# Kernel tuning notes

Hardware: AMD Instinct MI355X
Metric: run time of the kernel (lower is better)

## Reference

```python
import jax, jax.numpy as jnp
import numpy as np

LN_EPS = 1e-5

def layer_norm(x, w, b):
    mu = jnp.mean(x, axis=-1, keepdims=True)
    var = jnp.mean(jnp.square(x - mu), axis=-1, keepdims=True)
    return (x - mu) * jax.lax.rsqrt(var + LN_EPS) * w + b

def adaptive_mask_np(aa, bb, ada_para=0.2):
    # True = disallowed (matches torch ~bool mask). Static shapes -> numpy.
    adaptive_num = int(bb * ada_para)
    cc = bb // aa
    i = np.arange(aa)
    start = i * cc
    end = start + cc + adaptive_num
    over = end > bb - 1
    start = np.where(over, np.maximum(start - (end - (bb - 1)), 0), start)
    end = np.where(over, bb, end)
    cols = np.arange(bb)
    allowed = (cols[None, :] >= start[:, None]) & (cols[None, :] < end[:, None])
    return jnp.asarray(~allowed)  # [aa, bb] bool

def setup_inputs() -> dict:
    key = jax.random.key(0)
    ks = jax.random.split(key, 20)
    Lq, Lk, B, d, dff = 512, 4096, 4, 512, 2048
    s = lambda k, shape: jax.random.normal(k, shape, dtype=jnp.float32) * 0.02
    inp = {
        'tgt': jax.random.normal(ks[0], (Lq, B, d), dtype=jnp.float32),
        'memory': jax.random.normal(ks[1], (Lk, B, d), dtype=jnp.float32),
        'Wq': s(ks[2], (d, d)), 'bq': jnp.zeros((d,), jnp.float32),
        'Wk': s(ks[3], (d, d)), 'bk': jnp.zeros((d,), jnp.float32),
        'Wv': s(ks[4], (d, d)), 'bv': jnp.zeros((d,), jnp.float32),
        'Wo': s(ks[5], (d, d)), 'bo': jnp.zeros((d,), jnp.float32),
        'W1': s(ks[6], (dff, d)), 'b1': jnp.zeros((dff,), jnp.float32),
        'W2': s(ks[7], (d, dff)), 'b2': jnp.zeros((d,), jnp.float32),
        'ln1_w': jnp.ones((d,), jnp.float32), 'ln1_b': jnp.zeros((d,), jnp.float32),
        'ln2_w': jnp.ones((d,), jnp.float32), 'ln2_b': jnp.zeros((d,), jnp.float32),
        'ln3_w': jnp.ones((d,), jnp.float32), 'ln3_b': jnp.zeros((d,), jnp.float32),
        'ln4_w': jnp.ones((d,), jnp.float32), 'ln4_b': jnp.zeros((d,), jnp.float32),
    }
    return inp

def reference(tgt, memory, Wq, bq, Wk, bk, Wv, bv, Wo, bo, W1, b1, W2, b2,
              ln1_w, ln1_b, ln2_w, ln2_b, ln3_w, ln3_b, ln4_w, ln4_b):
    Lq, B, d = tgt.shape
    Lk = memory.shape[0]
    H = 8
    hd = d // H
    scale = 1.0 / jnp.sqrt(jnp.asarray(hd, tgt.dtype))

    t = layer_norm(tgt, ln1_w, ln1_b)      # [Lq,B,d]
    m = layer_norm(memory, ln2_w, ln2_b)   # [Lk,B,d]

    mask = adaptive_mask_np(Lq, Lk, 0.2)   # [Lq,Lk] bool, True=masked

    q = (t @ Wq.T + bq).reshape(Lq, B, H, hd)
    k = (m @ Wk.T + bk).reshape(Lk, B, H, hd)
    v = (m @ Wv.T + bv).reshape(Lk, B, H, hd)

    scores = jnp.einsum('qbhd,kbhd->bhqk', q * scale, k)
    scores = jnp.where(mask[None, None], -jnp.inf, scores)
    p = jax.nn.softmax(scores, axis=-1)                   # [B,H,Lq,Lk]
    attn_weights = jnp.mean(p, axis=1)                    # [B,Lq,Lk] (avg over heads)

    ctx = jnp.einsum('bhqk,kbhd->qbhd', p, v).reshape(Lq, B, d)
    tgt2 = ctx @ Wo.T + bo

    x = t + tgt2                       # dropout1 = identity (eval)
    x = layer_norm(x, ln3_w, ln3_b)
    ff = jax.nn.relu(x @ W1.T + b1) @ W2.T + b2
    x = x + ff                         # dropout2 = identity (eval)
    x = layer_norm(x, ln4_w, ln4_b)
    return (x, attn_weights)
```

## Files before the change

### kernel.cpp

```cpp
#include <hip/hip_runtime.h>
#include <hip/hip_bf16.h>

typedef __hip_bfloat16 bf16_t;
typedef __bf16 bf16x8 __attribute__((ext_vector_type(8)));
typedef float f32x4 __attribute__((ext_vector_type(4)));

#define LQ 512
#define LK 4096
#define BATCH 4
#define DMODEL 512
#define NHEAD 8
#define HEADDIM 64
#define DFF 2048
#define LN_EPS 1e-5f

#define KSTR 2080
#define VSTR 4128

__device__ inline float tofl(float x) { return x; }
__device__ inline float tofl(bf16_t x) { return __bfloat162float(x); }
__device__ inline void stfl(float* p, float v) { *p = v; }
__device__ inline void stfl(bf16_t* p, float v) { *p = __float2bfloat16(v); }

__device__ __forceinline__ void gld_lds16(const bf16_t* g, void* lds_base) {
    __builtin_amdgcn_global_load_lds(
        (const __attribute__((address_space(1))) uint32_t*)g,
        (__attribute__((address_space(3))) uint32_t*)lds_base, 16, 0, 0);
}

__global__ void prep_kernel(const float* __restrict__ s0, const float* __restrict__ s1,
                            const float* __restrict__ s2, const float* __restrict__ s3,
                            const float* __restrict__ s4,
                            bf16_t* __restrict__ wqkvo, bf16_t* __restrict__ w1bf) {
    int t = blockIdx.x * 256 + threadIdx.x;
    int which = t >> 16;
    int idx = (t & 65535) * 4;
    const float* s; bf16_t* d;
    if (which < 4) {
        s = (which == 0 ? s0 : which == 1 ? s1 : which == 2 ? s2 : s3);
        d = wqkvo + (size_t)which * 262144;
    } else {
        s = s4 + (size_t)(which - 4) * 262144;
        d = w1bf + (size_t)(which - 4) * 262144;
    }
    float4 v = *(const float4*)(s + idx);
    d[idx + 0] = __float2bfloat16(v.x);
    d[idx + 1] = __float2bfloat16(v.y);
    d[idx + 2] = __float2bfloat16(v.z);
    d[idx + 3] = __float2bfloat16(v.w);
}

__global__ void conv_w2(const float* __restrict__ s, bf16_t* __restrict__ d) {
    int i = (blockIdx.x * 256 + threadIdx.x) * 4;
    float4 v = *(const float4*)(s + i);
    d[i + 0] = __float2bfloat16(v.x);
    d[i + 1] = __float2bfloat16(v.y);
    d[i + 2] = __float2bfloat16(v.z);
    d[i + 3] = __float2bfloat16(v.w);
}

template <typename TOUT, bool DUAL>
__global__ void ln_kernel(const float* __restrict__ in, const float* __restrict__ w,
                          const float* __restrict__ b, TOUT* __restrict__ out1,
                          float* __restrict__ out2) {
    __shared__ float red[256];
    const int row = blockIdx.x;
    const int tid = threadIdx.x;
    const float* x = in + (size_t)row * DMODEL;
    float v0 = x[tid];
    float v1 = x[tid + 256];

    red[tid] = v0 + v1;
    __syncthreads();
    for (int s = 128; s > 0; s >>= 1) { if (tid < s) red[tid] += red[tid + s]; __syncthreads(); }
    float mu = red[0] * (1.0f / DMODEL);
    __syncthreads();

    float d0 = v0 - mu, d1 = v1 - mu;
    red[tid] = d0 * d0 + d1 * d1;
    __syncthreads();
    for (int s = 128; s > 0; s >>= 1) { if (tid < s) red[tid] += red[tid + s]; __syncthreads(); }
    float inv = rsqrtf(red[0] * (1.0f / DMODEL) + LN_EPS);

    float r0 = d0 * inv * w[tid] + b[tid];
    float r1 = d1 * inv * w[tid + 256] + b[tid + 256];
    TOUT* o = out1 + (size_t)row * DMODEL;
    stfl(&o[tid], r0);
    stfl(&o[tid + 256], r1);
    if (DUAL) {
        float* o2 = out2 + (size_t)row * DMODEL;
        o2[tid] = r0;
        o2[tid + 256] = r1;
    }
}

__global__ void ln12_kernel(const float* __restrict__ tgt, const float* __restrict__ memory,
                            const float* __restrict__ w1, const float* __restrict__ b1,
                            const float* __restrict__ w2, const float* __restrict__ b2,
                            bf16_t* __restrict__ t_bf, float* __restrict__ t_f32,
                            bf16_t* __restrict__ m_buf) {
    __shared__ float red[256];
    const int row = blockIdx.x;
    const int tid = threadIdx.x;
    const float* in; const float* w; const float* b;
    bf16_t* o1; float* o2; bool dual;
    if (row < 2048) {
        in = tgt + (size_t)row * DMODEL; w = w1; b = b1;
        o1 = t_bf + (size_t)row * DMODEL; o2 = t_f32 + (size_t)row * DMODEL; dual = true;
    } else {
        int r2 = row - 2048;
        in = memory + (size_t)r2 * DMODEL; w = w2; b = b2;
        o1 = m_buf + (size_t)r2 * DMODEL; o2 = nullptr; dual = false;
    }
    float v0 = in[tid];
    float v1 = in[tid + 256];
    red[tid] = v0 + v1;
    __syncthreads();
    for (int s = 128; s > 0; s >>= 1) { if (tid < s) red[tid] += red[tid + s]; __syncthreads(); }
    float mu = red[0] * (1.0f / DMODEL);
    __syncthreads();
    float d0 = v0 - mu, d1 = v1 - mu;
    red[tid] = d0 * d0 + d1 * d1;
    __syncthreads();
    for (int s = 128; s > 0; s >>= 1) { if (tid < s) red[tid] += red[tid + s]; __syncthreads(); }
    float inv = rsqrtf(red[0] * (1.0f / DMODEL) + LN_EPS);
    float r0 = d0 * inv * w[tid] + b[tid];
    float r1 = d1 * inv * w[tid + 256] + b[tid + 256];
    o1[tid] = __float2bfloat16(r0);
    o1[tid + 256] = __float2bfloat16(r1);
    if (dual) {
        o2[tid] = r0;
        o2[tid + 256] = r1;
    }
}

template <int TN, typename TC, bool RELU, bool RESID, bool KREMAP = false>
__global__ __launch_bounds__(256) void gemm_mfma(
        const bf16_t* __restrict__ A, const bf16_t* __restrict__ B,
        const float* __restrict__ bias, const float* __restrict__ resid,
        TC* __restrict__ C, int M, int N, int K) {
    __shared__ uint4 As4[1024];
    __shared__ uint4 Bs4[TN * 8];

    const int tid = threadIdx.x;
    const int lane = tid & 63;
    const int wave = tid >> 6;
    const int row16 = lane & 15;
    const int quad = lane >> 4;
    const int n0 = blockIdx.x * TN;
    const int m0 = blockIdx.y * 128;

    constexpr int MI = (TN == 128) ? 4 : 2;
    const int wy = (TN == 128) ? (wave >> 1) : wave;
    const int wx = (TN == 128) ? (wave & 1) : 0;
    const int m_base = wy * ((TN == 128) ? 64 : 32);
    const int n_base = wx * 64;

    const int rr = lane >> 3;
    const int kc = (lane & 7) ^ rr;
    const int kx = row16 & 7;

    const bf16_t* AsE = (const bf16_t*)As4;
    const bf16_t* BsE = (const bf16_t*)Bs4;

    f32x4 acc[MI][4] = {};

    for (int k0 = 0; k0 < K; k0 += 64) {
#pragma unroll
        for (int it = 0; it < 4; it++) {
            int issue = it * 4 + wave;
            int r = issue * 8 + rr;
            gld_lds16(A + (size_t)(m0 + r) * K + k0 + kc * 8, &As4[issue * 64]);
        }
#pragma unroll
        for (int it = 0; it < TN / 32; it++) {
            int issue = it * 4 + wave;
            int r = issue * 8 + rr;
            gld_lds16(B + (size_t)(n0 + r) * K + k0 + kc * 8, &Bs4[issue * 64]);
        }
        __syncthreads();
#pragma unroll
        for (int s = 0; s < 2; s++) {
            const int kq = s * 4 + quad;
            const int kcs = (kq ^ kx) * 8;
            bf16x8 af[MI], bfr[4];
#pragma unroll
            for (int i = 0; i < MI; i++)
                af[i] = *(const bf16x8*)&AsE[(m_base + i * 16 + row16) * 64 + kcs];
#pragma unroll
            for (int j = 0; j < 4; j++)
                bfr[j] = *(const bf16x8*)&BsE[(n_base + j * 16 + row16) * 64 + kcs];
#pragma unroll
            for (int i = 0; i < MI; i++)
#pragma unroll
                for (int j = 0; j < 4; j++)
                    acc[i][j] = __builtin_amdgcn_mfma_f32_16x16x32_bf16(af[i], bfr[j], acc[i][j], 0, 0, 0);
        }
        __syncthreads();
    }

#pragma unroll
    for (int i = 0; i < MI; i++) {
#pragma unroll
        for (int j = 0; j < 4; j++) {
            int col = n0 + n_base + j * 16 + row16;
            float bsv = bias[col];
#pragma unroll
            for (int r = 0; r < 4; r++) {
                int row = m0 + m_base + i * 16 + quad * 4 + r;
                float val = acc[i][j][r] + bsv;
                if (RESID) val += resid[(size_t)row * N + col];
                if (RELU) val = fmaxf(val, 0.0f);
                size_t caddr = KREMAP
                    ? ((size_t)(row >> 2) * KSTR + (size_t)(row & 3) * 512 + col)
                    : ((size_t)row * N + col);
                stfl(&C[caddr], val);
            }
        }
    }
}

__global__ __launch_bounds__(256) void transpose_kv(const bf16_t* __restrict__ kb,
                                                    bf16_t* __restrict__ kT) {
    __shared__ bf16_t tile[64][80];
    const int kt = blockIdx.x * 64;
    const int ct = blockIdx.y * 64;
    const int b  = blockIdx.z;
    const int t = threadIdx.x;
    {
        int kl = t >> 2, cl = (t & 3) * 16;
        const bf16_t* src = kb + ((size_t)(kt + kl) * 4 + b) * 512 + ct + cl;
        *(uint4*)&tile[kl][cl]     = *(const uint4*)src;
        *(uint4*)&tile[kl][cl + 8] = *(const uint4*)(src + 8);
    }
    __syncthreads();
    {
        int cl2 = t >> 2, ks = (t & 3) * 16;
        __attribute__((aligned(16))) bf16_t vals[16];
#pragma unroll
        for (int j = 0; j < 16; j++) vals[j] = tile[ks + j][cl2];
        bf16_t* dst = kT + ((size_t)b * 512 + ct + cl2) * VSTR + kt + ks;
        *(uint4*)dst       = *(const uint4*)&vals[0];
        *(uint4*)(dst + 8) = *(const uint4*)&vals[8];
    }
}

__device__ __forceinline__ void qk_issue(const bf16_t* kb_base, int us, int g,
                                         int row16, bf16x8 (&b0)[8], bf16x8 (&b1)[8]) {
#pragma unroll
    for (int j = 0; j < 8; ++j) {
        int key = us + (g * 8 + j) * 16 + row16;
        int key_eff = key > 4095 ? 4095 : key;
        const bf16_t* kr = kb_base + (size_t)key_eff * KSTR;
        b0[j] = *(const bf16x8*)kr;
        b1[j] = *(const bf16x8*)(kr + 32);
    }
}

__device__ __forceinline__ void qk_compute(int g, bf16x8 (&b0)[8], bf16x8 (&b1)[8],
        const bf16x8 aq0, const bf16x8 aq1, float (&l)[4], bf16_t* PsH,
        int row16, int quad, const int (&sq)[4], const int (&eq)[4], int us) {
#pragma unroll
    for (int j = 0; j < 8; ++j) {
        int it = g * 8 + j;
        f32x4 acc = {};
        acc = __builtin_amdgcn_mfma_f32_16x16x32_bf16(aq0, b0[j], acc, 0, 0, 0);
        acc = __builtin_amdgcn_mfma_f32_16x16x32_bf16(aq1, b1[j], acc, 0, 0, 0);
        int key = us + it * 16 + row16;
#pragma unroll
        for (int r = 0; r < 4; r++) {
            int ql = quad * 4 + r;
            bool valid = (key >= sq[r]) && (key < eq[r]);
            float p = valid ? __expf(0.125f * acc[r]) : 0.0f;
            l[r] += p;
            if (ql < 8) PsH[ql * 904 + it * 16 + row16] = __float2bfloat16(p);
        }
    }
}

__device__ __forceinline__ void pv_issue(const bf16_t* vbase, int g, int row16, int quad,
                                         bf16x8 (&vb)[4][4]) {
#pragma unroll
    for (int j = 0; j < 4; ++j) {
        int it = g * 4 + j;
#pragma unroll
        for (int nt = 0; nt < 4; ++nt)
            vb[j][nt] = *(const bf16x8*)(vbase + (size_t)(nt * 16 + row16) * VSTR
                                         + it * 32 + quad * 8);
    }
}

__device__ __forceinline__ void pv_compute(int g, bf16x8 (&vb)[4][4], const bf16_t* PsH,
        const bf16_t* Zrow, int row16, int quad, f32x4 (&o)[4]) {
#pragma unroll
    for (int j = 0; j < 4; ++j) {
        int it = g * 4 + j;
        const bf16_t* ap_src = (row16 < 8) ? &PsH[row16 * 904 + it * 32 + quad * 8]
                                           : &Zrow[0];
        bf16x8 ap = *(const bf16x8*)ap_src;
#pragma unroll
        for (int nt = 0; nt < 4; ++nt)
            o[nt] = __builtin_amdgcn_mfma_f32_16x16x32_bf16(ap, vb[j][nt], o[nt], 0, 0, 0);
    }
}

__global__ __launch_bounds__(512, 1) void attn_mfma(
        const bf16_t* __restrict__ qb,
        const bf16_t* __restrict__ kb,
        const bf16_t* __restrict__ vT,
        bf16_t* __restrict__ ctx,
        float* __restrict__ attn_out) {
    extern __shared__ char smem[];
    bf16_t* Ps   = (bf16_t*)smem;
    bf16_t* Qs   = (bf16_t*)(smem + 115712);
    bf16_t* Zrow = (bf16_t*)(smem + 115712 + 8320);
    float*  Ls   = (float*)(smem + 115712 + 8320 + 1808);

    const int blk = blockIdx.x;
    const int b  = (blk & 7) >> 1;
    const int qt = ((blk >> 3) << 1) | (blk & 1);
    const int q0 = qt * 8;
    const int tid = threadIdx.x;
    const int lane = tid & 63;
    const int h = tid >> 6;
    const int hoffg = h * HEADDIM;
    const int row16 = lane & 15;
    const int quad = lane >> 4;

    int us; { int s = q0 * 8, e = s + 827; if (e > 4095) s = 3268; us = s; }
    int sq[4], eq[4];
#pragma unroll
    for (int r = 0; r < 4; r++) {
        int ql = quad * 4 + r;
        if (ql < 8) {
            int s = (q0 + ql) * 8, e = s + 827;
            if (e > 4095) { s = 3268; e = 4096; }
            sq[r] = s; eq[r] = e;
        } else { sq[r] = 0; eq[r] = 0; }
    }

    {
        int r = tid >> 6, coff = (tid & 63) * 8;
        *(uint4*)&Qs[r * 520 + coff] =
            *(const uint4*)(qb + ((size_t)(q0 + r) * 4 + b) * 512 + coff);
        if (tid < 113) { uint4 z = {0, 0, 0, 0}; *(uint4*)&Zrow[tid * 8] = z; }
    }
    __syncthreads();

    const bf16_t* q0p = (row16 < 8) ? &Qs[row16 * 520 + hoffg + quad * 8] : &Zrow[0];
    const bf16_t* q1p = (row16 < 8) ? &Qs[row16 * 520 + hoffg + 32 + quad * 8] : &Zrow[8];
    const bf16x8 aq0 = *(const bf16x8*)q0p;
    const bf16x8 aq1 = *(const bf16x8*)q1p;

    bf16_t* PsH = Ps + h * 8 * 904;
    const bf16_t* kb_base = kb + b * 512 + hoffg + quad * 8;

    bf16x8 ka0[8], ka1[8], kc0[8], kc1[8];
    float l[4] = {0.f, 0.f, 0.f, 0.f};
    qk_issue(kb_base, us, 0, row16, ka0, ka1);
    for (int gg = 0; gg < 3; ++gg) {
        qk_issue(kb_base, us, 2 * gg + 1, row16, kc0, kc1);
        qk_compute(2 * gg, ka0, ka1, aq0, aq1, l, PsH, row16, quad, sq, eq, us);
        qk_issue(kb_base, us, 2 * gg + 2, row16, ka0, ka1);
        qk_compute(2 * gg + 1, kc0, kc1, aq0, aq1, l, PsH, row16, quad, sq, eq, us);
    }
    bf16x8 va[4][4], vb_[4][4];
    const bf16_t* vbase = vT + (size_t)(b * 512 + hoffg) * VSTR + us;
    pv_issue(vbase, 0, row16, quad, va);
    qk_compute(6, ka0, ka1, aq0, aq1, l, PsH, row16, quad, sq, eq, us);

#pragma unroll
    for (int off = 1; off < 16; off <<= 1) {
#pragma unroll
        for (int r = 0; r < 4; r++) l[r] += __shfl_xor(l[r], off, 64);
    }
    float linv[4];
#pragma unroll
    for (int r = 0; r < 4; r++) linv[r] = 1.0f / l[r];
    if (row16 == 0) {
#pragma unroll
        for (int r = 0; r < 4; r++) {
            int ql = quad * 4 + r;
            if (ql < 8) Ls[h * 8 + ql] = linv[r];
        }
    }

    f32x4 o[4] = {};
    for (int gg = 0; gg < 3; ++gg) {
        pv_issue(vbase, 2 * gg + 1, row16, quad, vb_);
        pv_compute(2 * gg, va, PsH, Zrow, row16, quad, o);
        pv_issue(vbase, 2 * gg + 2, row16, quad, va);
        pv_compute(2 * gg + 1, vb_, PsH, Zrow, row16, quad, o);
    }
    pv_compute(6, va, PsH, Zrow, row16, quad, o);

    __syncthreads();

    {
        int qq = h;
        float ls[8];
#pragma unroll
        for (int hh = 0; hh < 8; ++hh) ls[hh] = 0.125f * Ls[hh * 8 + qq];
        float* rowp = attn_out + ((size_t)b * LQ + q0 + qq) * LK;
        const bf16_t* ps = Ps + qq * 904;
        for (int it = 0; it < 16; ++it) {
            int c4 = (it * 64 + lane) * 4;
            float4 v = {0.f, 0.f, 0.f, 0.f};
            int off = c4 - us;
            if (off >= -3 && off < 896) {
#pragma unroll
                for (int e = 0; e < 4; ++e) {
                    int pc = off + e;
                    float s = 0.f;
                    if (pc >= 0 && pc < 896) {
#pragma unroll
                        for (int hh = 0; hh < 8; ++hh)
                            s += ls[hh] * tofl(ps[hh * 8 * 904 + pc]);
                    }
                    (&v.x)[e] = s;
                }
            }
            *(float4*)(rowp + c4) = v;
        }
    }

#pragma unroll
    for (int nt = 0; nt < 4; nt++) {
#pragma unroll
        for (int r = 0; r < 4; r++) {
            int ql = quad * 4 + r;
            if (ql < 8) {
                ctx[((size_t)(q0 + ql) * 4 + b) * 512 + hoffg + nt * 16 + row16] =
                    __float2bfloat16(o[nt][r] * linv[r]);
            }
        }
    }
}

extern "C" void kernel_launch(void* const* d_in, const int* in_sizes, int n_in,
                              void* d_out, int out_size, void* d_ws, size_t ws_size,
                              hipStream_t stream) {
    const float* tgt    = (const float*)d_in[0];
    const float* memory = (const float*)d_in[1];
    const float* Wq = (const float*)d_in[2];
    const float* bq = (const float*)d_in[3];
    const float* Wk = (const float*)d_in[4];
    const float* bk = (const float*)d_in[5];
    const float* Wv = (const float*)d_in[6];
    const float* bv = (const float*)d_in[7];
    const float* Wo = (const float*)d_in[8];
    const float* bo = (const float*)d_in[9];
    const float* W1 = (const float*)d_in[10];
    const float* b1 = (const float*)d_in[11];
    const float* W2 = (const float*)d_in[12];
    const float* b2 = (const float*)d_in[13];
    const float* ln1w = (const float*)d_in[14];
    const float* ln1b = (const float*)d_in[15];
    const float* ln2w = (const float*)d_in[16];
    const float* ln2b = (const float*)d_in[17];
    const float* ln3w = (const float*)d_in[18];
    const float* ln3b = (const float*)d_in[19];
    const float* ln4w = (const float*)d_in[20];
    const float* ln4b = (const float*)d_in[21];

    const size_t M1 = (size_t)LQ * BATCH;
    const size_t M2 = (size_t)LK * BATCH;
    const size_t SZ1 = M1 * DMODEL;

    char* wsb = (char*)d_ws;
    const size_t MB = 1 << 20;
    bf16_t* m_buf   = (bf16_t*)(wsb + 0 * MB);
    bf16_t* vT_buf  = (bf16_t*)(wsb + 0 * MB);
    bf16_t* h_buf   = (bf16_t*)(wsb + 0 * MB);
    bf16_t* k_buf   = (bf16_t*)(wsb + 17 * MB);
    float*  xres    = (float*)(wsb + 17 * MB);
    float*  xln_f   = (float*)(wsb + 21 * MB);
    float*  x2_buf  = (float*)(wsb + 25 * MB);
    bf16_t* W2_bf   = (bf16_t*)(wsb + 34 * MB);
    bf16_t* v_buf   = (bf16_t*)(wsb + 34 * MB);
    bf16_t* t_bf    = (bf16_t*)(wsb + 50 * MB);
    bf16_t* xln_bf  = (bf16_t*)(wsb + 50 * MB);
    float*  t_f32   = (float*)(wsb + 52 * MB);
    bf16_t* q_bf    = (bf16_t*)(wsb + 56 * MB);
    bf16_t* ctx_buf = (bf16_t*)(wsb + 58 * MB);
    bf16_t* wqkvo   = (bf16_t*)(wsb + 60 * MB);
    bf16_t* W1_bf   = (bf16_t*)(wsb + 62 * MB);

    bf16_t* Wq_bf = wqkvo;
    bf16_t* Wk_bf = wqkvo + 262144;
    bf16_t* Wv_bf = wqkvo + 2 * 262144;
    bf16_t* Wo_bf = wqkvo + 3 * 262144;

    float* out_x    = (float*)d_out;
    float* out_attn = out_x + SZ1;

    prep_kernel<<<dim3(2048), dim3(256), 0, stream>>>(
        Wq, Wk, Wv, Wo, W1, wqkvo, W1_bf);

    ln12_kernel<<<dim3(M1 + M2), dim3(256), 0, stream>>>(
        tgt, memory, ln1w, ln1b, ln2w, ln2b, t_bf, t_f32, m_buf);

    gemm_mfma<64, bf16_t, false, false><<<dim3(8, 16), dim3(256), 0, stream>>>(
        t_bf, Wq_bf, bq, nullptr, q_bf, M1, DMODEL, DMODEL);
    gemm_mfma<128, bf16_t, false, false, true><<<dim3(4, 128), dim3(256), 0, stream>>>(
        m_buf, Wk_bf, bk, nullptr, k_buf, M2, DMODEL, DMODEL);
    gemm_mfma<128, bf16_t, false, false><<<dim3(4, 128), dim3(256), 0, stream>>>(
        m_buf, Wv_bf, bv, nullptr, v_buf, M2, DMODEL, DMODEL);

    transpose_kv<<<dim3(64, 8, 4), dim3(256), 0, stream>>>(v_buf, vT_buf);

    conv_w2<<<dim3(1024), dim3(256), 0, stream>>>(W2, W2_bf);

    const int attn_lds = 115712 + 8320 + 1808 + 256;
    hipFuncSetAttribute((const void*)attn_mfma,
                        hipFuncAttributeMaxDynamicSharedMemorySize, attn_lds);
    attn_mfma<<<dim3(256), dim3(512), attn_lds, stream>>>(
        q_bf, k_buf, vT_buf, ctx_buf, out_attn);

    gemm_mfma<64, float, false, true><<<dim3(8, 16), dim3(256), 0, stream>>>(
        ctx_buf, Wo_bf, bo, t_f32, xres, M1, DMODEL, DMODEL);

    ln_kernel<bf16_t, true><<<dim3(M1), dim3(256), 0, stream>>>(xres, ln3w, ln3b, xln_bf, xln_f);

    gemm_mfma<128, bf16_t, true, false><<<dim3(16, 16), dim3(256), 0, stream>>>(
        xln_bf, W1_bf, b1, nullptr, h_buf, M1, DFF, DMODEL);

    gemm_mfma<64, float, false, true><<<dim3(8, 16), dim3(256), 0, stream>>>(
        h_buf, W2_bf, b2, xln_f, x2_buf, M1, DMODEL, DFF);

    ln_kernel<float, false><<<dim3(M1), dim3(256), 0, stream>>>(x2_buf, ln4w, ln4b, out_x, nullptr);
}
```

Measured before the change: 305.8 us.

## Fuse K and V projections into one GEMM and triple-buffer attention loads

Replaces the two separate K and V projection GEMM launches with one kernel. It loads each A tile of the normalized memory once and computes both K and V outputs from it, which halves the A-side global traffic and removes one launch. The attention kernel also moves from double to triple buffering of K and V register fragments, issuing loads two stages ahead to hide more latency. The cost is higher register pressure in both kernels (two accumulator sets in the GEMM, three fragment buffers in attention), which could reduce occupancy or cause spills.

```diff
diff --git a/kernel.cpp b/kernel.cpp
--- a/kernel.cpp
+++ b/kernel.cpp
@@ -220,6 +220,101 @@
     }
 }
 
+__global__ __launch_bounds__(256, 1) void gemm_kv(
+        const bf16_t* __restrict__ A, const bf16_t* __restrict__ BK,
+        const bf16_t* __restrict__ BV, const float* __restrict__ biask,
+        const float* __restrict__ biasv, bf16_t* __restrict__ CK,
+        bf16_t* __restrict__ CV, int M, int N, int K) {
+    __shared__ uint4 As4[1024];
+    __shared__ uint4 BKs4[1024];
+    __shared__ uint4 BVs4[1024];
+
+    const int tid = threadIdx.x;
+    const int lane = tid & 63;
+    const int wave = tid >> 6;
+    const int row16 = lane & 15;
+    const int quad = lane >> 4;
+    const int n0 = blockIdx.x * 128;
+    const int m0 = blockIdx.y * 128;
+
+    const int wy = wave >> 1;
+    const int wx = wave & 1;
+    const int m_base = wy * 64;
+    const int n_base = wx * 64;
+
+    const int rr = lane >> 3;
+    const int kc = (lane & 7) ^ rr;
+    const int kx = row16 & 7;
+
+    const bf16_t* AsE = (const bf16_t*)As4;
+    const bf16_t* BKsE = (const bf16_t*)BKs4;
+    const bf16_t* BVsE = (const bf16_t*)BVs4;
+
+    f32x4 accK[4][4] = {};
+    f32x4 accV[4][4] = {};
+
+    for (int k0 = 0; k0 < K; k0 += 64) {
+#pragma unroll
+        for (int it = 0; it < 4; it++) {
+            int issue = it * 4 + wave;
+            int r = issue * 8 + rr;
+            gld_lds16(A + (size_t)(m0 + r) * K + k0 + kc * 8, &As4[issue * 64]);
+        }
+#pragma unroll
+        for (int it = 0; it < 4; it++) {
+            int issue = it * 4 + wave;
+            int r = issue * 8 + rr;
+            gld_lds16(BK + (size_t)(n0 + r) * K + k0 + kc * 8, &BKs4[issue * 64]);
+        }
+#pragma unroll
+        for (int it = 0; it < 4; it++) {
+            int issue = it * 4 + wave;
+            int r = issue * 8 + rr;
+            gld_lds16(BV + (size_t)(n0 + r) * K + k0 + kc * 8, &BVs4[issue * 64]);
+        }
+        __syncthreads();
+#pragma unroll
+        for (int s = 0; s < 2; s++) {
+            const int kq = s * 4 + quad;
+            const int kcs = (kq ^ kx) * 8;
+            bf16x8 af[4], bkf[4], bvf[4];
+#pragma unroll
+            for (int i = 0; i < 4; i++)
+                af[i] = *(const bf16x8*)&AsE[(m_base + i * 16 + row16) * 64 + kcs];
+#pragma unroll
+            for (int j = 0; j < 4; j++) {
+                bkf[j] = *(const bf16x8*)&BKsE[(n_base + j * 16 + row16) * 64 + kcs];
+                bvf[j] = *(const bf16x8*)&BVsE[(n_base + j * 16 + row16) * 64 + kcs];
+            }
+#pragma unroll
+            for (int i = 0; i < 4; i++)
+#pragma unroll
+                for (int j = 0; j < 4; j++) {
+                    accK[i][j] = __builtin_amdgcn_mfma_f32_16x16x32_bf16(af[i], bkf[j], accK[i][j], 0, 0, 0);
+                    accV[i][j] = __builtin_amdgcn_mfma_f32_16x16x32_bf16(af[i], bvf[j], accV[i][j], 0, 0, 0);
+                }
+        }
+        __syncthreads();
+    }
+
+#pragma unroll
+    for (int i = 0; i < 4; i++) {
+#pragma unroll
+        for (int j = 0; j < 4; j++) {
+            int col = n0 + n_base + j * 16 + row16;
+            float bk_ = biask[col];
+            float bv_ = biasv[col];
+#pragma unroll
+            for (int r = 0; r < 4; r++) {
+                int row = m0 + m_base + i * 16 + quad * 4 + r;
+                CK[(size_t)(row >> 2) * KSTR + (size_t)(row & 3) * 512 + col] =
+                    __float2bfloat16(accK[i][j][r] + bk_);
+                CV[(size_t)row * N + col] = __float2bfloat16(accV[i][j][r] + bv_);
+            }
+        }
+    }
+}
+
 __global__ __launch_bounds__(256) void transpose_kv(const bf16_t* __restrict__ kb,
                                                     bf16_t* __restrict__ kT) {
     __shared__ bf16_t tile[64][80];
@@ -355,19 +450,27 @@
     bf16_t* PsH = Ps + h * 8 * 904;
     const bf16_t* kb_base = kb + b * 512 + hoffg + quad * 8;
 
-    bf16x8 ka0[8], ka1[8], kc0[8], kc1[8];
+    bf16x8 kA0[8], kA1[8], kB0[8], kB1[8], kC0[8], kC1[8];
     float l[4] = {0.f, 0.f, 0.f, 0.f};
-    qk_issue(kb_base, us, 0, row16, ka0, ka1);
-    for (int gg = 0; gg < 3; ++gg) {
-        qk_issue(kb_base, us, 2 * gg + 1, row16, kc0, kc1);
-        qk_compute(2 * gg, ka0, ka1, aq0, aq1, l, PsH, row16, quad, sq, eq, us);
-        qk_issue(kb_base, us, 2 * gg + 2, row16, ka0, ka1);
-        qk_compute(2 * gg + 1, kc0, kc1, aq0, aq1, l, PsH, row16, quad, sq, eq, us);
-    }
-    bf16x8 va[4][4], vb_[4][4];
+    qk_issue(kb_base, us, 0, row16, kA0, kA1);
+    qk_issue(kb_base, us, 1, row16, kB0, kB1);
+    qk_compute(0, kA0, kA1, aq0, aq1, l, PsH, row16, quad, sq, eq, us);
+    qk_issue(kb_base, us, 2, row16, kC0, kC1);
+    qk_compute(1, kB0, kB1, aq0, aq1, l, PsH, row16, quad, sq, eq, us);
+    qk_issue(kb_base, us, 3, row16, kA0, kA1);
+    qk_compute(2, kC0, kC1, aq0, aq1, l, PsH, row16, quad, sq, eq, us);
+    qk_issue(kb_base, us, 4, row16, kB0, kB1);
+    qk_compute(3, kA0, kA1, aq0, aq1, l, PsH, row16, quad, sq, eq, us);
+    qk_issue(kb_base, us, 5, row16, kC0, kC1);
+    qk_compute(4, kB0, kB1, aq0, aq1, l, PsH, row16, quad, sq, eq, us);
+    qk_issue(kb_base, us, 6, row16, kA0, kA1);
+
+    bf16x8 vA[4][4], vB[4][4], vC[4][4];
     const bf16_t* vbase = vT + (size_t)(b * 512 + hoffg) * VSTR + us;
-    pv_issue(vbase, 0, row16, quad, va);
-    qk_compute(6, ka0, ka1, aq0, aq1, l, PsH, row16, quad, sq, eq, us);
+    pv_issue(vbase, 0, row16, quad, vA);
+    qk_compute(5, kC0, kC1, aq0, aq1, l, PsH, row16, quad, sq, eq, us);
+    pv_issue(vbase, 1, row16, quad, vB);
+    qk_compute(6, kA0, kA1, aq0, aq1, l, PsH, row16, quad, sq, eq, us);
 
 #pragma unroll
     for (int off = 1; off < 16; off <<= 1) {
@@ -386,13 +489,18 @@
     }
 
     f32x4 o[4] = {};
-    for (int gg = 0; gg < 3; ++gg) {
-        pv_issue(vbase, 2 * gg + 1, row16, quad, vb_);
-        pv_compute(2 * gg, va, PsH, Zrow, row16, quad, o);
-        pv_issue(vbase, 2 * gg + 2, row16, quad, va);
-        pv_compute(2 * gg + 1, vb_, PsH, Zrow, row16, quad, o);
-    }
-    pv_compute(6, va, PsH, Zrow, row16, quad, o);
+    pv_issue(vbase, 2, row16, quad, vC);
+    pv_compute(0, vA, PsH, Zrow, row16, quad, o);
+    pv_issue(vbase, 3, row16, quad, vA);
+    pv_compute(1, vB, PsH, Zrow, row16, quad, o);
+    pv_issue(vbase, 4, row16, quad, vB);
+    pv_compute(2, vC, PsH, Zrow, row16, quad, o);
+    pv_issue(vbase, 5, row16, quad, vC);
+    pv_compute(3, vA, PsH, Zrow, row16, quad, o);
+    pv_issue(vbase, 6, row16, quad, vA);
+    pv_compute(4, vB, PsH, Zrow, row16, quad, o);
+    pv_compute(5, vC, PsH, Zrow, row16, quad, o);
+    pv_compute(6, vA, PsH, Zrow, row16, quad, o);
 
     __syncthreads();
 
@@ -502,10 +610,9 @@
 
     gemm_mfma<64, bf16_t, false, false><<<dim3(8, 16), dim3(256), 0, stream>>>(
         t_bf, Wq_bf, bq, nullptr, q_bf, M1, DMODEL, DMODEL);
-    gemm_mfma<128, bf16_t, false, false, true><<<dim3(4, 128), dim3(256), 0, stream>>>(
-        m_buf, Wk_bf, bk, nullptr, k_buf, M2, DMODEL, DMODEL);
-    gemm_mfma<128, bf16_t, false, false><<<dim3(4, 128), dim3(256), 0, stream>>>(
-        m_buf, Wv_bf, bv, nullptr, v_buf, M2, DMODEL, DMODEL);
+
+    gemm_kv<<<dim3(4, 128), dim3(256), 0, stream>>>(
+        m_buf, Wk_bf, Wv_bf, bk, bv, k_buf, v_buf, M2, DMODEL, DMODEL);
 
     transpose_kv<<<dim3(64, 8, 4), dim3(256), 0, stream>>>(v_buf, vT_buf);
 
```

Result: slower. 379.1 us (+23.9%).

## Add 64x64-tile GEMM for small projections and raise MFMA priority in attention

Applied to the files above, without the earlier changes.

Adds a new gemm64 kernel with 64x64 output tiles, so the Q, output-projection and W2 GEMMs (M=2048) launch 256 blocks instead of 128 and use more of the GPU's compute units. It also wraps the QK and PV MFMA compute sections of the attention kernel in s_setprio(1)/s_setprio(0), so waves doing matrix math get scheduling priority over waves issuing loads. The smaller tiles mean less data reuse per block and more loads of A and B overall.

```diff
diff --git a/kernel.cpp b/kernel.cpp
--- a/kernel.cpp
+++ b/kernel.cpp
@@ -220,6 +220,88 @@
     }
 }
 
+template <typename TC, bool RELU, bool RESID>
+__global__ __launch_bounds__(256) void gemm64(
+        const bf16_t* __restrict__ A, const bf16_t* __restrict__ B,
+        const float* __restrict__ bias, const float* __restrict__ resid,
+        TC* __restrict__ C, int M, int N, int K) {
+    __shared__ uint4 As4[512];
+    __shared__ uint4 Bs4[512];
+
+    const int tid = threadIdx.x;
+    const int lane = tid & 63;
+    const int wave = tid >> 6;
+    const int row16 = lane & 15;
+    const int quad = lane >> 4;
+    const int n0 = blockIdx.x * 64;
+    const int m0 = blockIdx.y * 64;
+
+    const int wy = wave >> 1;
+    const int wx = wave & 1;
+    const int m_base = wy * 32;
+    const int n_base = wx * 32;
+
+    const int rr = lane >> 3;
+    const int kc = (lane & 7) ^ rr;
+    const int kx = row16 & 7;
+
+    const bf16_t* AsE = (const bf16_t*)As4;
+    const bf16_t* BsE = (const bf16_t*)Bs4;
+
+    f32x4 acc[2][2] = {};
+
+    for (int k0 = 0; k0 < K; k0 += 64) {
+#pragma unroll
+        for (int it = 0; it < 2; it++) {
+            int issue = it * 4 + wave;
+            int r = issue * 8 + rr;
+            gld_lds16(A + (size_t)(m0 + r) * K + k0 + kc * 8, &As4[issue * 64]);
+        }
+#pragma unroll
+        for (int it = 0; it < 2; it++) {
+            int issue = it * 4 + wave;
+            int r = issue * 8 + rr;
+            gld_lds16(B + (size_t)(n0 + r) * K + k0 + kc * 8, &Bs4[issue * 64]);
+        }
+        __syncthreads();
+#pragma unroll
+        for (int s = 0; s < 2; s++) {
+            const int kq = s * 4 + quad;
+            const int kcs = (kq ^ kx) * 8;
+            bf16x8 af[2], bfr[2];
+#pragma unroll
+            for (int i = 0; i < 2; i++)
+                af[i] = *(const bf16x8*)&AsE[(m_base + i * 16 + row16) * 64 + kcs];
+#pragma unroll
+            for (int j = 0; j < 2; j++)
+                bfr[j] = *(const bf16x8*)&BsE[(n_base + j * 16 + row16) * 64 + kcs];
+#pragma unroll
+            for (int i = 0; i < 2; i++)
+#pragma unroll
+                for (int j = 0; j < 2; j++)
+                    acc[i][j] = __builtin_amdgcn_mfma_f32_16x16x32_bf16(af[i], bfr[j], acc[i][j], 0, 0, 0);
+        }
+        __syncthreads();
+    }
+
+#pragma unroll
+    for (int i = 0; i < 2; i++) {
+#pragma unroll
+        for (int j = 0; j < 2; j++) {
+            int col = n0 + n_base + j * 16 + row16;
+            float bsv = bias[col];
+#pragma unroll
+            for (int r = 0; r < 4; r++) {
+                int row = m0 + m_base + i * 16 + quad * 4 + r;
+                float val = acc[i][j][r] + bsv;
+                if (RESID) val += resid[(size_t)row * N + col];
+                if (RELU) val = fmaxf(val, 0.0f);
+                stfl(&C[(size_t)row * N + col], val);
+            }
+        }
+    }
+}
+
 __global__ __launch_bounds__(256) void transpose_kv(const bf16_t* __restrict__ kb,
                                                     bf16_t* __restrict__ kT) {
     __shared__ bf16_t tile[64][80];
@@ -260,6 +342,7 @@
 __device__ __forceinline__ void qk_compute(int g, bf16x8 (&b0)[8], bf16x8 (&b1)[8],
         const bf16x8 aq0, const bf16x8 aq1, float (&l)[4], bf16_t* PsH,
         int row16, int quad, const int (&sq)[4], const int (&eq)[4], int us) {
+    __builtin_amdgcn_s_setprio(1);
 #pragma unroll
     for (int j = 0; j < 8; ++j) {
         int it = g * 8 + j;
@@ -276,6 +359,7 @@
             if (ql < 8) PsH[ql * 904 + it * 16 + row16] = __float2bfloat16(p);
         }
     }
+    __builtin_amdgcn_s_setprio(0);
 }
 
 __device__ __forceinline__ void pv_issue(const bf16_t* vbase, int g, int row16, int quad,
@@ -292,6 +376,7 @@
 
 __device__ __forceinline__ void pv_compute(int g, bf16x8 (&vb)[4][4], const bf16_t* PsH,
         const bf16_t* Zrow, int row16, int quad, f32x4 (&o)[4]) {
+    __builtin_amdgcn_s_setprio(1);
 #pragma unroll
     for (int j = 0; j < 4; ++j) {
         int it = g * 4 + j;
@@ -302,6 +387,7 @@
         for (int nt = 0; nt < 4; ++nt)
             o[nt] = __builtin_amdgcn_mfma_f32_16x16x32_bf16(ap, vb[j][nt], o[nt], 0, 0, 0);
     }
+    __builtin_amdgcn_s_setprio(0);
 }
 
 __global__ __launch_bounds__(512, 1) void attn_mfma(
@@ -500,8 +586,9 @@
     ln12_kernel<<<dim3(M1 + M2), dim3(256), 0, stream>>>(
         tgt, memory, ln1w, ln1b, ln2w, ln2b, t_bf, t_f32, m_buf);
 
-    gemm_mfma<64, bf16_t, false, false><<<dim3(8, 16), dim3(256), 0, stream>>>(
+    gemm64<bf16_t, false, false><<<dim3(8, 32), dim3(256), 0, stream>>>(
         t_bf, Wq_bf, bq, nullptr, q_bf, M1, DMODEL, DMODEL);
+
     gemm_mfma<128, bf16_t, false, false, true><<<dim3(4, 128), dim3(256), 0, stream>>>(
         m_buf, Wk_bf, bk, nullptr, k_buf, M2, DMODEL, DMODEL);
     gemm_mfma<128, bf16_t, false, false><<<dim3(4, 128), dim3(256), 0, stream>>>(
@@ -517,7 +604,7 @@
     attn_mfma<<<dim3(256), dim3(512), attn_lds, stream>>>(
         q_bf, k_buf, vT_buf, ctx_buf, out_attn);
 
-    gemm_mfma<64, float, false, true><<<dim3(8, 16), dim3(256), 0, stream>>>(
+    gemm64<float, false, true><<<dim3(8, 32), dim3(256), 0, stream>>>(
         ctx_buf, Wo_bf, bo, t_f32, xres, M1, DMODEL, DMODEL);
 
     ln_kernel<bf16_t, true><<<dim3(M1), dim3(256), 0, stream>>>(xres, ln3w, ln3b, xln_bf, xln_f);
@@ -525,7 +612,7 @@
     gemm_mfma<128, bf16_t, true, false><<<dim3(16, 16), dim3(256), 0, stream>>>(
         xln_bf, W1_bf, b1, nullptr, h_buf, M1, DFF, DMODEL);
 
-    gemm_mfma<64, float, false, true><<<dim3(8, 16), dim3(256), 0, stream>>>(
+    gemm64<float, false, true><<<dim3(8, 32), dim3(256), 0, stream>>>(
         h_buf, W2_bf, b2, xln_f, x2_buf, M1, DMODEL, DFF);
 
     ln_kernel<float, false><<<dim3(M1), dim3(256), 0, stream>>>(x2_buf, ln4w, ln4b, out_x, nullptr);
```

Result: faster. 294.3 us (-3.8%).
